# Performance work log

Hardware: AMD Instinct MI355X
Metric: run time of the kernel (lower is better)

## Reference

```python
import jax, jax.numpy as jnp
import numpy as np

T, B, E, H = 1024, 8, 512, 8
D = E // H  # head_dim = 64
SCALE = D ** -0.5


def setup_inputs() -> dict:
    key = jax.random.key(0)
    ks = jax.random.split(key, 6)
    w_scale = 0.02  # xavier-ish small init so softmax is not saturated
    return {
        "query_r": jax.random.normal(ks[0], (T, B, E), jnp.float32),
        "query_i": jax.random.normal(ks[1], (T, B, E), jnp.float32),
        "W_qkv_r": jax.random.normal(ks[2], (3 * E, E), jnp.float32) * w_scale,
        "W_qkv_i": jax.random.normal(ks[3], (3 * E, E), jnp.float32) * w_scale,
        "b_qkv_r": jnp.zeros((3 * E,), jnp.float32),
        "b_qkv_i": jnp.zeros((3 * E,), jnp.float32),
        "W_out_r": jax.random.normal(ks[4], (E, E), jnp.float32) * w_scale,
        "W_out_i": jax.random.normal(ks[5], (E, E), jnp.float32) * w_scale,
        "b_out_r": jnp.zeros((E,), jnp.float32),
        "b_out_i": jnp.zeros((E,), jnp.float32),
    }


def _complex_linear(x_r, x_i, W_r, W_i, b_r, b_i):
    # ComplexLinear: (Wr + i Wi)(xr + i xi) + (br + i bi), Linear weight is [out,in]
    y_r = x_r @ W_r.T - x_i @ W_i.T + b_r
    y_i = x_i @ W_r.T + x_r @ W_i.T + b_i
    return y_r, y_i


def _heads(x):
    # [T, B, E] -> [B*H, T, D]  (matches view(T, B*H, D).transpose(0,1))
    return x.reshape(T, B * H, D).transpose(1, 0, 2)


def reference(query_r, query_i, W_qkv_r, W_qkv_i, b_qkv_r, b_qkv_i,
              W_out_r, W_out_i, b_out_r, b_out_i):
    qkv_r, qkv_i = _complex_linear(query_r, query_i, W_qkv_r, W_qkv_i, b_qkv_r, b_qkv_i)
    q_r, k_r, v_r = jnp.split(qkv_r, 3, axis=-1)
    q_i, k_i, v_i = jnp.split(qkv_i, 3, axis=-1)
    q_r, q_i = _heads(q_r), _heads(q_i)
    k_r, k_i = _heads(k_r), _heads(k_i)
    v_r, v_i = _heads(v_r), _heads(v_i)

    # qk_inner = q @ conj(k)^T  (complex)
    s_rr = jnp.einsum('btd,bsd->bts', q_r, k_r)
    s_ii = jnp.einsum('btd,bsd->bts', q_i, k_i)
    s_ir = jnp.einsum('btd,bsd->bts', q_i, k_r)
    s_ri = jnp.einsum('btd,bsd->bts', q_r, k_i)
    aw_r = jax.nn.softmax((s_rr + s_ii) * SCALE, axis=-1)
    aw_i = jax.nn.softmax((s_ir - s_ri) * SCALE, axis=-1)

    # attn = attn_weights @ conj(v)
    attn_r = jnp.einsum('bts,bsd->btd', aw_r, v_r) + jnp.einsum('bts,bsd->btd', aw_i, v_i)
    attn_i = jnp.einsum('bts,bsd->btd', aw_i, v_r) - jnp.einsum('bts,bsd->btd', aw_r, v_i)

    # [B*H, T, D] -> [T, B, E]
    attn_r = attn_r.transpose(1, 0, 2).reshape(T, B, E)
    attn_i = attn_i.transpose(1, 0, 2).reshape(T, B, E)
    out_r, out_i = _complex_linear(attn_r, attn_i, W_out_r, W_out_i, b_out_r, b_out_i)

    # averaged attention weights over heads (complex), returned as real/imag stack
    aw_avg_r = aw_r.reshape(B, H, T, T).mean(axis=1)
    aw_avg_i = aw_i.reshape(B, H, T, T).mean(axis=1)
    return jnp.stack([out_r, out_i]), jnp.stack([aw_avg_r, aw_avg_i])
```

## Files before the change

kernel.cpp:

```cpp
#include <hip/hip_runtime.h>
#include <math.h>

#define TT 1024
#define BB 8
#define EE 512
#define HH 8
#define DD 64
#define MM (TT*BB)
#define NQKV (3*EE)

typedef _Float16 f16;
typedef f16 f16x8 __attribute__((ext_vector_type(8)));
typedef f16 f16x4 __attribute__((ext_vector_type(4)));
typedef float f32x4 __attribute__((ext_vector_type(4)));

#define MFMA16 __builtin_amdgcn_mfma_f32_16x16x32_f16

typedef __attribute__((address_space(3))) void lds_t;
typedef const __attribute__((address_space(1))) void gmem_t;
__device__ inline void gld_lds16(const void* g, void* l) {
    __builtin_amdgcn_global_load_lds((gmem_t*)g, (lds_t*)l, 16, 0, 0);
}

typedef const __attribute__((address_space(3))) f16 lds_cf16;
__device__ inline f16x4 tr16(const void* p) {
    f16x4 d;
    asm volatile("ds_read_b64_tr_b16 %0, %1" : "=v"(d) : "v"((lds_cf16*)p));
    return d;
}

__global__ __launch_bounds__(256) void cvt_f16_pair(
    const float* __restrict__ sr, const float* __restrict__ si,
    f16* __restrict__ dr, f16* __restrict__ di, int n4)
{
    const int idx = blockIdx.x * 256 + threadIdx.x;
    if (idx < n4) {
        const float4 a = ((const float4*)sr)[idx];
        const float4 b = ((const float4*)si)[idx];
        f16x4 fa, fb;
        fa[0]=(f16)a.x; fa[1]=(f16)a.y; fa[2]=(f16)a.z; fa[3]=(f16)a.w;
        fb[0]=(f16)b.x; fb[1]=(f16)b.y; fb[2]=(f16)b.z; fb[3]=(f16)b.w;
        ((f16x4*)dr)[idx] = fa;
        ((f16x4*)di)[idx] = fb;
    }
}

__global__ __launch_bounds__(256, 2) void gemm_cplx_f16(
    const f16* __restrict__ Xr, const f16* __restrict__ Xi,
    const f16* __restrict__ Wr, const f16* __restrict__ Wi,
    const float* __restrict__ biasr, const float* __restrict__ biasi,
    void* __restrict__ Yr_, void* __restrict__ Yi_,
    int N, int K, int storef16)
{
    __shared__ __attribute__((aligned(16))) f16 Asr[128][32];
    __shared__ __attribute__((aligned(16))) f16 Asi[128][32];
    __shared__ __attribute__((aligned(16))) f16 Bsr[128][32];
    __shared__ __attribute__((aligned(16))) f16 Bsi[128][32];

    const int tid  = threadIdx.x;
    const int wave = tid >> 6;
    const int lane = tid & 63;
    const int c16  = lane & 15;
    const int g    = lane >> 4;
    const int wm = wave >> 1, wn = wave & 1;
    const int m0 = blockIdx.y * 128;
    const int n0 = blockIdx.x * 128;

    const int srow = tid >> 2;
    const int sseg = tid & 3;

    f32x4 accr[4][4] = {};
    f32x4 acci[4][4] = {};

    for (int k0 = 0; k0 < K; k0 += 32) {
        __syncthreads();
        #pragma unroll
        for (int is = 0; is < 2; ++is) {
            const int row = is * 64 + srow;
            const size_t xb = (size_t)(m0 + row) * K + k0 + sseg * 8;
            const size_t wb = (size_t)(n0 + row) * K + k0 + sseg * 8;
            const int dof = is * 4096 + wave * 1024;
            gld_lds16(Xr + xb, (char*)Asr + dof);
            gld_lds16(Xi + xb, (char*)Asi + dof);
            gld_lds16(Wr + wb, (char*)Bsr + dof);
            gld_lds16(Wi + wb, (char*)Bsi + dof);
        }
        __syncthreads();

        f16x8 a_r[4], a_i[4], na_i[4];
        #pragma unroll
        for (int mi = 0; mi < 4; ++mi) {
            const int row = wm * 64 + mi * 16 + c16;
            a_r[mi] = *(const f16x8*)((const char*)Asr + row * 64 + g * 16);
            a_i[mi] = *(const f16x8*)((const char*)Asi + row * 64 + g * 16);
            na_i[mi] = -a_i[mi];
        }
        #pragma unroll
        for (int ni = 0; ni < 4; ++ni) {
            const int row = wn * 64 + ni * 16 + c16;
            const f16x8 b_r = *(const f16x8*)((const char*)Bsr + row * 64 + g * 16);
            const f16x8 b_i = *(const f16x8*)((const char*)Bsi + row * 64 + g * 16);
            #pragma unroll
            for (int mi = 0; mi < 4; ++mi) {
                accr[mi][ni] = MFMA16(a_r[mi],  b_r, accr[mi][ni], 0,0,0);
                accr[mi][ni] = MFMA16(na_i[mi], b_i, accr[mi][ni], 0,0,0);
                acci[mi][ni] = MFMA16(a_i[mi],  b_r, acci[mi][ni], 0,0,0);
                acci[mi][ni] = MFMA16(a_r[mi],  b_i, acci[mi][ni], 0,0,0);
            }
        }
    }

    float biasR[4], biasI[4];
    #pragma unroll
    for (int ni = 0; ni < 4; ++ni) {
        const int n = n0 + wn * 64 + ni * 16 + c16;
        biasR[ni] = biasr[n];
        biasI[ni] = biasi[n];
    }
    #pragma unroll
    for (int mi = 0; mi < 4; ++mi) {
        #pragma unroll
        for (int ni = 0; ni < 4; ++ni) {
            const int n = n0 + wn * 64 + ni * 16 + c16;
            #pragma unroll
            for (int rg = 0; rg < 4; ++rg) {
                const size_t m = (size_t)(m0 + wm * 64 + mi * 16 + g * 4 + rg);
                const float vr = accr[mi][ni][rg] + biasR[ni];
                const float vi = acci[mi][ni][rg] + biasI[ni];
                if (storef16) {
                    ((f16*)Yr_)[m * N + n] = (f16)vr;
                    ((f16*)Yi_)[m * N + n] = (f16)vi;
                } else {
                    ((float*)Yr_)[m * N + n] = vr;
                    ((float*)Yi_)[m * N + n] = vi;
                }
            }
        }
    }
}

__global__ __launch_bounds__(256, 2) void attn_mfma10(
    const f16* __restrict__ qkv_r, const f16* __restrict__ qkv_i,
    f16* __restrict__ attn_r, f16* __restrict__ attn_i,
    float* __restrict__ aw_out)
{
    __shared__ __attribute__((aligned(16))) char S[65536];
    __shared__ __attribute__((aligned(16))) char VR[16384];

    const int blk = blockIdx.x;
    const int b  = blk & 7;
    const int qt = blk >> 3;
    const int t0 = qt * 16;
    const int tid = threadIdx.x;
    const int wave = tid >> 6, lane = tid & 63;
    const int c16 = lane & 15, g = lane >> 4;
    const int r = tid >> 4, c = tid & 15;

    f16x8 acc8[2][8] = {};

    const int vkey = (lane >> 1) & 31;
    const int vdl  = (lane & 1) * 8;
    char* ring = VR + wave * 1024;

    f16x8 sc8;
    #pragma unroll
    for (int e = 0; e < 8; ++e) sc8[e] = (f16)0.125f;

    for (int h = 0; h < HH; ++h) {
        const size_t qoff = ((size_t)(t0 + c16) * BB + b) * NQKV + h * DD;
        const f16x8 qr0 = *(const f16x8*)(qkv_r + qoff + g * 8)      * sc8;
        const f16x8 qr1 = *(const f16x8*)(qkv_r + qoff + 32 + g * 8) * sc8;
        const f16x8 qi0 = *(const f16x8*)(qkv_i + qoff + g * 8)      * sc8;
        const f16x8 qi1 = *(const f16x8*)(qkv_i + qoff + 32 + g * 8) * sc8;
        const f16x8 nqr0 = -qr0, nqr1 = -qr1;

        #pragma unroll 2
        for (int ch = 0; ch < 16; ++ch) {
            const int key = ch * 64 + wave * 16 + c16;
            const size_t kb = ((size_t)key * BB + b) * NQKV + EE + h * DD;
            const f16x8 kr0 = *(const f16x8*)(qkv_r + kb + g * 8);
            const f16x8 kr1 = *(const f16x8*)(qkv_r + kb + 32 + g * 8);
            const f16x8 ki0 = *(const f16x8*)(qkv_i + kb + g * 8);
            const f16x8 ki1 = *(const f16x8*)(qkv_i + kb + 32 + g * 8);
            f32x4 sr = {}, si = {};
            sr = MFMA16(kr0, qr0, sr, 0,0,0); sr = MFMA16(kr1, qr1, sr, 0,0,0);
            sr = MFMA16(ki0, qi0, sr, 0,0,0); sr = MFMA16(ki1, qi1, sr, 0,0,0);
            si = MFMA16(kr0, qi0, si, 0,0,0); si = MFMA16(kr1, qi1, si, 0,0,0);
            si = MFMA16(ki0, nqr0, si, 0,0,0); si = MFMA16(ki1, nqr1, si, 0,0,0);
            const int key0 = ch * 64 + wave * 16 + g * 4;
            f16x4 s4r, s4i;
            #pragma unroll
            for (int e = 0; e < 4; ++e) { s4r[e] = (f16)sr[e]; s4i[e] = (f16)si[e]; }
            const int off = c16 * 2048 + ((key0 * 2) ^ ((c16 & 7) << 4));
            *(f16x4*)(S + off)         = s4r;
            *(f16x4*)(S + 32768 + off) = s4i;
        }
        __syncthreads();

        {
            const size_t vb0 = ((size_t)vkey * BB + b) * NQKV + 2*EE + h*DD
                             + wave * 16 + vdl;
            gld_lds16(qkv_r + vb0, ring);
            gld_lds16(qkv_i + vb0, ring + 4096);
            const size_t vb1 = ((size_t)(32 + vkey) * BB + b) * NQKV + 2*EE + h*DD
                             + wave * 16 + vdl;
            gld_lds16(qkv_r + vb1, ring + 8192);
            gld_lds16(qkv_i + vb1, ring + 8192 + 4096);
        }

        #pragma unroll
        for (int p = 0; p < 2; ++p) {
            char* rowb = S + p * 32768 + r * 2048;
            const int sw = (r & 7) << 4;
            f16x8 v[8];
            #pragma unroll
            for (int i = 0; i < 8; ++i)
                v[i] = *(const f16x8*)(rowb + (((c * 8 + i * 128) * 2) ^ sw));
            f16x8 m8 = v[0];
            #pragma unroll
            for (int i = 1; i < 8; ++i) {
                #pragma unroll
                for (int e = 0; e < 8; ++e)
                    m8[e] = (v[i][e] > m8[e]) ? v[i][e] : m8[e];
            }
            float m = -1e30f;
            #pragma unroll
            for (int e = 0; e < 8; ++e) m = fmaxf(m, (float)m8[e]);
            #pragma unroll
            for (int off = 8; off; off >>= 1) m = fmaxf(m, __shfl_xor(m, off, 16));
            float sum = 0.f;
            #pragma unroll
            for (int i = 0; i < 8; ++i) {
                f16x8 ev;
                #pragma unroll
                for (int e = 0; e < 8; ++e) {
                    const float x = __expf((float)v[i][e] - m);
                    ev[e] = (f16)x;
                    sum += x;
                }
                v[i] = ev;
            }
            #pragma unroll
            for (int off = 8; off; off >>= 1) sum += __shfl_xor(sum, off, 16);
            const f16 invh = (f16)(1.0f / sum);
            f16x8 inv8;
            #pragma unroll
            for (int e = 0; e < 8; ++e) inv8[e] = invh;
            #pragma unroll
            for (int i = 0; i < 8; ++i) {
                const f16x8 av = v[i] * inv8;
                *(f16x8*)(rowb + (((c * 8 + i * 128) * 2) ^ sw)) = av;
                acc8[p][i] += av;
            }
        }
        __syncthreads();

        f32x4 pr0 = {}, pr1 = {}, pi0 = {}, pi1 = {};
        const int arow = c16 * 2048;
        const int asw = (c16 & 7) << 4;
        #pragma unroll 2
        for (int hf = 0; hf < 32; ++hf) {
            const int slot = hf & 1;
            if (hf < 31) asm volatile("s_waitcnt vmcnt(2)" ::: "memory");
            else         asm volatile("s_waitcnt vmcnt(0)" ::: "memory");
            const char* vbase = ring + slot * 8192 + g * 256 + c16 * 8;
            const f16x4 vr_lo = tr16(vbase);
            const f16x4 vr_hi = tr16(vbase + 128);
            const f16x4 vi_lo = tr16(vbase + 4096);
            const f16x4 vi_hi = tr16(vbase + 4096 + 128);
            const int j0 = hf * 32 + g * 8;
            const f16x8 awr = *(const f16x8*)(S + arow + ((j0 * 2) ^ asw));
            const f16x8 awi = *(const f16x8*)(S + 32768 + arow + ((j0 * 2) ^ asw));
            asm volatile("s_waitcnt lgkmcnt(0)" ::: "memory");
            __builtin_amdgcn_sched_barrier(0);
            if (hf + 2 < 32) {
                const size_t vb = ((size_t)((hf + 2) * 32 + vkey) * BB + b) * NQKV
                                + 2*EE + h*DD + wave * 16 + vdl;
                gld_lds16(qkv_r + vb, ring + slot * 8192);
                gld_lds16(qkv_i + vb, ring + slot * 8192 + 4096);
            }
            const f16x8 vr8 = __builtin_shufflevector(vr_lo, vr_hi, 0,1,2,3,4,5,6,7);
            const f16x8 vi8 = __builtin_shufflevector(vi_lo, vi_hi, 0,1,2,3,4,5,6,7);
            const f16x8 nvi8 = -vi8;
            if (slot) {
                pr1 = MFMA16(awr, vr8,  pr1, 0,0,0);
                pr1 = MFMA16(awi, vi8,  pr1, 0,0,0);
                pi1 = MFMA16(awi, vr8,  pi1, 0,0,0);
                pi1 = MFMA16(awr, nvi8, pi1, 0,0,0);
            } else {
                pr0 = MFMA16(awr, vr8,  pr0, 0,0,0);
                pr0 = MFMA16(awi, vi8,  pr0, 0,0,0);
                pi0 = MFMA16(awi, vr8,  pi0, 0,0,0);
                pi0 = MFMA16(awr, nvi8, pi0, 0,0,0);
            }
        }
        const f32x4 pr = pr0 + pr1, pi = pi0 + pi1;
        __syncthreads();

        #pragma unroll
        for (int rg = 0; rg < 4; ++rg) {
            const int q = g * 4 + rg;
            const int d = wave * 16 + c16;
            const size_t ob = ((size_t)(t0 + q) * BB + b) * EE + h * DD + d;
            attn_r[ob] = (f16)pr[rg];
            attn_i[ob] = (f16)pi[rg];
        }
    }

    #pragma unroll
    for (int p = 0; p < 2; ++p) {
        float* dst = aw_out + (size_t)p * BB * TT * TT + ((size_t)b * TT + t0 + r) * TT;
        #pragma unroll
        for (int i = 0; i < 8; ++i) {
            const int j = c * 8 + i * 128;
            float4 v0, v1;
            v0.x = (float)acc8[p][i][0] * 0.125f; v0.y = (float)acc8[p][i][1] * 0.125f;
            v0.z = (float)acc8[p][i][2] * 0.125f; v0.w = (float)acc8[p][i][3] * 0.125f;
            v1.x = (float)acc8[p][i][4] * 0.125f; v1.y = (float)acc8[p][i][5] * 0.125f;
            v1.z = (float)acc8[p][i][6] * 0.125f; v1.w = (float)acc8[p][i][7] * 0.125f;
            *(float4*)(dst + j) = v0;
            *(float4*)(dst + j + 4) = v1;
        }
    }
}

extern "C" void kernel_launch(void* const* d_in, const int* in_sizes, int n_in,
                              void* d_out, int out_size, void* d_ws, size_t ws_size,
                              hipStream_t stream)
{
    const float* query_r = (const float*)d_in[0];
    const float* query_i = (const float*)d_in[1];
    const float* W_qkv_r = (const float*)d_in[2];
    const float* W_qkv_i = (const float*)d_in[3];
    const float* b_qkv_r = (const float*)d_in[4];
    const float* b_qkv_i = (const float*)d_in[5];
    const float* W_out_r = (const float*)d_in[6];
    const float* W_out_i = (const float*)d_in[7];
    const float* b_out_r = (const float*)d_in[8];
    const float* b_out_i = (const float*)d_in[9];

    char* w = (char*)d_ws;
    f16* q16_r = (f16*)(w);
    f16* q16_i = (f16*)(w + 8388608);
    f16* Wq_r  = (f16*)(w + 16777216);
    f16* Wq_i  = (f16*)(w + 18350080);
    f16* Wo_r  = (f16*)(w + 19922944);
    f16* Wo_i  = (f16*)(w + 20447232);
    f16* qkv_r = (f16*)(w + 20971520);
    f16* qkv_i = (f16*)(w + 46137344);
    f16* at_r  = (f16*)(w + 71303168);
    f16* at_i  = (f16*)(w + 79691776);

    float* out   = (float*)d_out;
    float* out_r = out;
    float* out_i = out + (size_t)MM * EE;
    float* aw    = out + 2 * (size_t)MM * EE;

    {
        const int n4q = MM * EE / 4;
        cvt_f16_pair<<<dim3((n4q + 255) / 256), dim3(256), 0, stream>>>(
            query_r, query_i, q16_r, q16_i, n4q);
        const int n4wq = NQKV * EE / 4;
        cvt_f16_pair<<<dim3((n4wq + 255) / 256), dim3(256), 0, stream>>>(
            W_qkv_r, W_qkv_i, Wq_r, Wq_i, n4wq);
        const int n4wo = EE * EE / 4;
        cvt_f16_pair<<<dim3((n4wo + 255) / 256), dim3(256), 0, stream>>>(
            W_out_r, W_out_i, Wo_r, Wo_i, n4wo);
    }
    gemm_cplx_f16<<<dim3(NQKV / 128, MM / 128), dim3(256), 0, stream>>>(
        q16_r, q16_i, Wq_r, Wq_i, b_qkv_r, b_qkv_i,
        (void*)qkv_r, (void*)qkv_i, NQKV, EE, 1);
    attn_mfma10<<<dim3(TT / 16 * BB), dim3(256), 0, stream>>>(
        qkv_r, qkv_i, at_r, at_i, aw);
    gemm_cplx_f16<<<dim3(EE / 128, MM / 128), dim3(256), 0, stream>>>(
        at_r, at_i, Wo_r, Wo_i, b_out_r, b_out_i,
        (void*)out_r, (void*)out_i, EE, EE, 0);
}
```

Measured before the change: 343.1 us.

## Pre-transpose V into a key-contiguous layout and load it directly in attention

Adds a separate kernel that transposes V into a [B, E, T] layout, so each attention lane can read 8 consecutive keys straight from global memory. This replaces the LDS ring buffer, the async global-to-LDS loads, the waitcnt pipelining and the ds_read_b64_tr_b16 transposed reads in the PV loop. The aim is to simplify the PV stage and free LDS. In exchange it adds a kernel launch plus an extra write and read of V (about 16 MB), and the direct global loads in the PV loop are no longer explicitly prefetched.

```diff
diff --git a/kernel.cpp b/kernel.cpp
--- a/kernel.cpp
+++ b/kernel.cpp
@@ -20,13 +20,6 @@
 typedef const __attribute__((address_space(1))) void gmem_t;
 __device__ inline void gld_lds16(const void* g, void* l) {
     __builtin_amdgcn_global_load_lds((gmem_t*)g, (lds_t*)l, 16, 0, 0);
-}
-
-typedef const __attribute__((address_space(3))) f16 lds_cf16;
-__device__ inline f16x4 tr16(const void* p) {
-    f16x4 d;
-    asm volatile("ds_read_b64_tr_b16 %0, %1" : "=v"(d) : "v"((lds_cf16*)p));
-    return d;
 }
 
 __global__ __launch_bounds__(256) void cvt_f16_pair(
@@ -42,6 +35,43 @@
         fb[0]=(f16)b.x; fb[1]=(f16)b.y; fb[2]=(f16)b.z; fb[3]=(f16)b.w;
         ((f16x4*)dr)[idx] = fa;
         ((f16x4*)di)[idx] = fb;
+    }
+}
+
+__global__ __launch_bounds__(256) void transpose_v(
+    const f16* __restrict__ qkv_r, const f16* __restrict__ qkv_i,
+    f16* __restrict__ vTr, f16* __restrict__ vTi)
+{
+    __shared__ f16 L[64][68];
+    const int e0 = blockIdx.x * 64;
+    const int t0 = blockIdx.y * 64;
+    const int b  = blockIdx.z;
+    const int tid = threadIdx.x;
+    #pragma unroll
+    for (int p = 0; p < 2; ++p) {
+        const f16* src = p ? qkv_i : qkv_r;
+        f16* dst = p ? vTi : vTr;
+        if (p) __syncthreads();
+        #pragma unroll
+        for (int pass = 0; pass < 4; ++pass) {
+            const int idx = pass * 256 + tid;
+            const int t = idx >> 4;
+            const int c = (idx & 15) * 4;
+            const f16x4 v = *(const f16x4*)(src +
+                ((size_t)(t0 + t) * BB + b) * NQKV + 2 * EE + e0 + c);
+            *(f16x4*)&L[t][c] = v;
+        }
+        __syncthreads();
+        #pragma unroll
+        for (int pass = 0; pass < 4; ++pass) {
+            const int idx = pass * 256 + tid;
+            const int e = idx >> 4;
+            const int t4 = (idx & 15) * 4;
+            f16x4 v;
+            v[0] = L[t4 + 0][e]; v[1] = L[t4 + 1][e];
+            v[2] = L[t4 + 2][e]; v[3] = L[t4 + 3][e];
+            *(f16x4*)(dst + ((size_t)b * EE + e0 + e) * TT + t0 + t4) = v;
+        }
     }
 }
 
@@ -139,13 +169,13 @@
     }
 }
 
-__global__ __launch_bounds__(256, 2) void attn_mfma10(
+__global__ __launch_bounds__(256, 2) void attn_mfma11(
     const f16* __restrict__ qkv_r, const f16* __restrict__ qkv_i,
+    const f16* __restrict__ vTr, const f16* __restrict__ vTi,
     f16* __restrict__ attn_r, f16* __restrict__ attn_i,
     float* __restrict__ aw_out)
 {
     __shared__ __attribute__((aligned(16))) char S[65536];
-    __shared__ __attribute__((aligned(16))) char VR[16384];
 
     const int blk = blockIdx.x;
     const int b  = blk & 7;
@@ -157,10 +187,6 @@
     const int r = tid >> 4, c = tid & 15;
 
     f16x8 acc8[2][8] = {};
-
-    const int vkey = (lane >> 1) & 31;
-    const int vdl  = (lane & 1) * 8;
-    char* ring = VR + wave * 1024;
 
     f16x8 sc8;
     #pragma unroll
@@ -197,17 +223,6 @@
         }
         __syncthreads();
 
-        {
-            const size_t vb0 = ((size_t)vkey * BB + b) * NQKV + 2*EE + h*DD
-                             + wave * 16 + vdl;
-            gld_lds16(qkv_r + vb0, ring);
-            gld_lds16(qkv_i + vb0, ring + 4096);
-            const size_t vb1 = ((size_t)(32 + vkey) * BB + b) * NQKV + 2*EE + h*DD
-                             + wave * 16 + vdl;
-            gld_lds16(qkv_r + vb1, ring + 8192);
-            gld_lds16(qkv_i + vb1, ring + 8192 + 4096);
-        }
-
         #pragma unroll
         for (int p = 0; p < 2; ++p) {
             char* rowb = S + p * 32768 + r * 2048;
@@ -256,33 +271,20 @@
         __syncthreads();
 
         f32x4 pr0 = {}, pr1 = {}, pi0 = {}, pi1 = {};
+        const size_t vrow = ((size_t)b * EE + h * DD + wave * 16 + c16) * TT;
+        const f16* vr_row = vTr + vrow;
+        const f16* vi_row = vTi + vrow;
         const int arow = c16 * 2048;
         const int asw = (c16 & 7) << 4;
-        #pragma unroll 2
+        #pragma unroll 4
         for (int hf = 0; hf < 32; ++hf) {
-            const int slot = hf & 1;
-            if (hf < 31) asm volatile("s_waitcnt vmcnt(2)" ::: "memory");
-            else         asm volatile("s_waitcnt vmcnt(0)" ::: "memory");
-            const char* vbase = ring + slot * 8192 + g * 256 + c16 * 8;
-            const f16x4 vr_lo = tr16(vbase);
-            const f16x4 vr_hi = tr16(vbase + 128);
-            const f16x4 vi_lo = tr16(vbase + 4096);
-            const f16x4 vi_hi = tr16(vbase + 4096 + 128);
             const int j0 = hf * 32 + g * 8;
+            const f16x8 vr8 = *(const f16x8*)(vr_row + j0);
+            const f16x8 vi8 = *(const f16x8*)(vi_row + j0);
             const f16x8 awr = *(const f16x8*)(S + arow + ((j0 * 2) ^ asw));
             const f16x8 awi = *(const f16x8*)(S + 32768 + arow + ((j0 * 2) ^ asw));
-            asm volatile("s_waitcnt lgkmcnt(0)" ::: "memory");
-            __builtin_amdgcn_sched_barrier(0);
-            if (hf + 2 < 32) {
-                const size_t vb = ((size_t)((hf + 2) * 32 + vkey) * BB + b) * NQKV
-                                + 2*EE + h*DD + wave * 16 + vdl;
-                gld_lds16(qkv_r + vb, ring + slot * 8192);
-                gld_lds16(qkv_i + vb, ring + slot * 8192 + 4096);
-            }
-            const f16x8 vr8 = __builtin_shufflevector(vr_lo, vr_hi, 0,1,2,3,4,5,6,7);
-            const f16x8 vi8 = __builtin_shufflevector(vi_lo, vi_hi, 0,1,2,3,4,5,6,7);
             const f16x8 nvi8 = -vi8;
-            if (slot) {
+            if (hf & 1) {
                 pr1 = MFMA16(awr, vr8,  pr1, 0,0,0);
                 pr1 = MFMA16(awi, vi8,  pr1, 0,0,0);
                 pi1 = MFMA16(awi, vr8,  pi1, 0,0,0);
@@ -350,6 +352,8 @@
     f16* qkv_i = (f16*)(w + 46137344);
     f16* at_r  = (f16*)(w + 71303168);
     f16* at_i  = (f16*)(w + 79691776);
+    f16* vT_r  = (f16*)(w + 88080384);
+    f16* vT_i  = (f16*)(w + 96468992);
 
     float* out   = (float*)d_out;
     float* out_r = out;
@@ -370,8 +374,10 @@
     gemm_cplx_f16<<<dim3(NQKV / 128, MM / 128), dim3(256), 0, stream>>>(
         q16_r, q16_i, Wq_r, Wq_i, b_qkv_r, b_qkv_i,
         (void*)qkv_r, (void*)qkv_i, NQKV, EE, 1);
-    attn_mfma10<<<dim3(TT / 16 * BB), dim3(256), 0, stream>>>(
-        qkv_r, qkv_i, at_r, at_i, aw);
+    transpose_v<<<dim3(EE / 64, TT / 64, BB), dim3(256), 0, stream>>>(
+        qkv_r, qkv_i, vT_r, vT_i);
+    attn_mfma11<<<dim3(TT / 16 * BB), dim3(256), 0, stream>>>(
+        qkv_r, qkv_i, vT_r, vT_i, at_r, at_i, aw);
     gemm_cplx_f16<<<dim3(EE / 128, MM / 128), dim3(256), 0, stream>>>(
         at_r, at_i, Wo_r, Wo_i, b_out_r, b_out_i,
         (void*)out_r, (void*)out_i, EE, EE, 0);
```

Result: slower. 418.4 us (+21.9%).
